# Kernel optimization log

Measured on AMD Instinct MI355X. Metric: run time of the kernel, lower is better.

Reference implementation:

```python
import jax, jax.numpy as jnp
import numpy as np

N_SEGMENTS = 50000  # number of destination nodes (index values in [0, N_SEGMENTS))


def setup_inputs() -> dict:
    key = jax.random.key(0)
    k1, k2 = jax.random.split(key)
    input = jax.random.normal(k1, (1600000, 64), dtype=jnp.float32)
    index = jax.random.randint(k2, (1600000,), 0, N_SEGMENTS, dtype=jnp.int64)
    return {"input": input, "index": index}


def reference(input, index):
    # Sum-aggregate rows of `input` grouped by `index`: out[n] = sum_{e: index[e]==n} input[e]
    # Equivalent to the custom loma_sum_aggr forward (scatter-add segmented reduction).
    return jax.ops.segment_sum(input, index, num_segments=N_SEGMENTS)
```

## Files before the change

### kernel.cpp

```cpp
#include <hip/hip_runtime.h>
#include <hip/hip_bf16.h>

#define N_SEGMENTS 50000
#define N_ROWS     1600000
#define N_FEAT     64

__global__ void seg_sum_atomic(const float* __restrict__ in,
                               const int*   __restrict__ idx,
                               float*       __restrict__ out) {
    long long t   = (long long)blockIdx.x * blockDim.x + threadIdx.x;
    long long row = t >> 6;
    int       c   = (int)(t & 63);
    if (row < (long long)N_ROWS) {
        int s = idx[row];
        float v = in[row * N_FEAT + c];
        atomicAdd(out + (long long)s * N_FEAT + c, v);
    }
}

extern "C" void kernel_launch(void* const* d_in, const int* in_sizes, int n_in,
                              void* d_out, int out_size, void* d_ws, size_t ws_size,
                              hipStream_t stream) {
    const float* in  = (const float*)d_in[0];
    const int*   idx = (const int*)d_in[1];
    float*       out = (float*)d_out;

    hipMemsetAsync(d_out, 0, (size_t)out_size * sizeof(float), stream);

    const long long total = (long long)N_ROWS * N_FEAT;
    const int block = 256;
    const long long grid = (total + block - 1) / block;

    seg_sum_atomic<<<(unsigned)grid, block, 0, stream>>>(in, idx, out);
}
```

Baseline: 738.3 us.

## Replace atomic scatter-add with counting-sort CSR build and per-segment gather reduction

Builds a CSR grouping of rows by segment: a histogram, a single-block prefix scan, and a scatter of row ids via atomic cursors. A wave-per-segment gather kernel then sums each segment's rows in registers and writes the output once. This removes 102M float atomics and the output memset, at the cost of several extra launches, a serial single-block scan, and random-order row reads. It falls back to the atomic kernel if the workspace is too small.

```diff
diff --git a/kernel.cpp b/kernel.cpp
--- a/kernel.cpp
+++ b/kernel.cpp
@@ -1,5 +1,4 @@
 #include <hip/hip_runtime.h>
-#include <hip/hip_bf16.h>
 
 #define N_SEGMENTS 50000
 #define N_ROWS     1600000
@@ -18,6 +17,92 @@
     }
 }
 
+__global__ void hist_kernel(const int* __restrict__ idx, int* __restrict__ cnt) {
+    int t = blockIdx.x * blockDim.x + threadIdx.x;
+    int r = t << 2;
+    if (r < N_ROWS) {
+        int4 v = *reinterpret_cast<const int4*>(idx + r);
+        atomicAdd(&cnt[v.x], 1);
+        atomicAdd(&cnt[v.y], 1);
+        atomicAdd(&cnt[v.z], 1);
+        atomicAdd(&cnt[v.w], 1);
+    }
+}
+
+__global__ void __launch_bounds__(1024) scan_kernel(const int* __restrict__ cnt,
+                                                    int* __restrict__ base,
+                                                    int* __restrict__ cursor) {
+    __shared__ int part[1024];
+    int t = threadIdx.x;
+    const int CHUNK = (N_SEGMENTS + 1023) / 1024;
+    int lo = t * CHUNK;
+    int hi = lo + CHUNK; if (hi > N_SEGMENTS) hi = N_SEGMENTS;
+    if (lo > N_SEGMENTS) lo = N_SEGMENTS;
+    int sum = 0;
+    for (int i = lo; i < hi; ++i) sum += cnt[i];
+    part[t] = sum;
+    __syncthreads();
+    for (int ofs = 1; ofs < 1024; ofs <<= 1) {
+        int v = (t >= ofs) ? part[t - ofs] : 0;
+        __syncthreads();
+        part[t] += v;
+        __syncthreads();
+    }
+    int run = (t == 0) ? 0 : part[t - 1];
+    for (int i = lo; i < hi; ++i) {
+        base[i]   = run;
+        cursor[i] = run;
+        run += cnt[i];
+    }
+    if (t == 1023) base[N_SEGMENTS] = N_ROWS;
+}
+
+__global__ void scatter_kernel(const int* __restrict__ idx,
+                               int* __restrict__ cursor,
+                               int* __restrict__ rowids) {
+    int t = blockIdx.x * blockDim.x + threadIdx.x;
+    int r = t << 2;
+    if (r < N_ROWS) {
+        int4 v = *reinterpret_cast<const int4*>(idx + r);
+        rowids[atomicAdd(&cursor[v.x], 1)] = r;
+        rowids[atomicAdd(&cursor[v.y], 1)] = r + 1;
+        rowids[atomicAdd(&cursor[v.z], 1)] = r + 2;
+        rowids[atomicAdd(&cursor[v.w], 1)] = r + 3;
+    }
+}
+
+__global__ void gather_kernel(const float* __restrict__ in,
+                              const int*   __restrict__ rowids,
+                              const int*   __restrict__ base,
+                              float*       __restrict__ out) {
+    int wave = (blockIdx.x * blockDim.x + threadIdx.x) >> 6;
+    int lane = threadIdx.x & 63;
+    if (wave >= N_SEGMENTS) return;
+    int beg = base[wave];
+    int end = base[wave + 1];
+    float a0 = 0.f, a1 = 0.f, a2 = 0.f, a3 = 0.f;
+    for (int j0 = beg; j0 < end; j0 += 64) {
+        int n = end - j0; if (n > 64) n = 64;
+        int myid = (lane < n) ? rowids[j0 + lane] : 0;
+        int k = 0;
+        for (; k + 4 <= n; k += 4) {
+            int r0 = __shfl(myid, k);
+            int r1 = __shfl(myid, k + 1);
+            int r2 = __shfl(myid, k + 2);
+            int r3 = __shfl(myid, k + 3);
+            a0 += in[r0 * N_FEAT + lane];
+            a1 += in[r1 * N_FEAT + lane];
+            a2 += in[r2 * N_FEAT + lane];
+            a3 += in[r3 * N_FEAT + lane];
+        }
+        for (; k < n; ++k) {
+            int r = __shfl(myid, k);
+            a0 += in[r * N_FEAT + lane];
+        }
+    }
+    out[wave * N_FEAT + lane] = (a0 + a1) + (a2 + a3);
+}
+
 extern "C" void kernel_launch(void* const* d_in, const int* in_sizes, int n_in,
                               void* d_out, int out_size, void* d_ws, size_t ws_size,
                               hipStream_t stream) {
@@ -25,11 +110,29 @@
     const int*   idx = (const int*)d_in[1];
     float*       out = (float*)d_out;
 
-    hipMemsetAsync(d_out, 0, (size_t)out_size * sizeof(float), stream);
+    const size_t need = ((size_t)N_SEGMENTS * 3 + 1 + N_ROWS) * sizeof(int);
+    if (ws_size < need) {
+        hipMemsetAsync(d_out, 0, (size_t)out_size * sizeof(float), stream);
+        const long long total = (long long)N_ROWS * N_FEAT;
+        const int block = 256;
+        const long long grid = (total + block - 1) / block;
+        seg_sum_atomic<<<(unsigned)grid, block, 0, stream>>>(in, idx, out);
+        return;
+    }
 
-    const long long total = (long long)N_ROWS * N_FEAT;
+    int* cnt    = (int*)d_ws;
+    int* base   = cnt + N_SEGMENTS;
+    int* cursor = base + N_SEGMENTS + 1;
+    int* rowids = cursor + N_SEGMENTS;
+
+    hipMemsetAsync(cnt, 0, (size_t)N_SEGMENTS * sizeof(int), stream);
+
     const int block = 256;
-    const long long grid = (total + block - 1) / block;
+    const int gridRows = (N_ROWS / 4 + block - 1) / block;
+    hist_kernel   <<<gridRows, block, 0, stream>>>(idx, cnt);
+    scan_kernel   <<<1, 1024, 0, stream>>>(cnt, base, cursor);
+    scatter_kernel<<<gridRows, block, 0, stream>>>(idx, cursor, rowids);
 
-    seg_sum_atomic<<<(unsigned)grid, block, 0, stream>>>(in, idx, out);
+    const int gridGather = (N_SEGMENTS * 64) / 256;
+    gather_kernel <<<gridGather, block, 0, stream>>>(in, rowids, base, out);
 }
```

Result: slower. 842.8 us (+14.2%).
